# Optimization experiments

Measured on AMD Instinct MI355X. Metric: run time of the kernel, lower is better.

## Reference

```python
import jax, jax.numpy as jnp
import numpy as np

N = 100000
IN_F, C1, C2, C3, OUT_F = 64, 64, 64, 64, 8


def setup_inputs() -> dict:
    key = jax.random.key(0)
    ks = jax.random.split(key, 12)
    x = jax.random.normal(ks[0], (N, IN_F), dtype=jnp.float32)
    edge_index = jax.random.randint(ks[1], (2, 1600000), 0, N, dtype=jnp.int64)

    def lin(kw, kb, fi, fo):
        s = 1.0 / np.sqrt(fi)
        W = jax.random.uniform(kw, (fi, fo), jnp.float32, -s, s)
        b = jax.random.uniform(kb, (fo,), jnp.float32, -s, s)
        return W, b

    W1, b1 = lin(ks[2], ks[3], IN_F, C1)
    W2, b2 = lin(ks[4], ks[5], C1, C2)
    W3, b3 = lin(ks[6], ks[7], C2, C3)
    Wl, bl = lin(ks[8], ks[9], C3, OUT_F)
    return {"x": x, "edge_index": edge_index, "W1": W1, "b1": b1,
            "W2": W2, "b2": b2, "W3": W3, "b3": b3, "Wl": Wl, "bl": bl}


def _gcn_norm(edge_index, n):
    # add self loops, compute symmetric normalization D^-1/2 A D^-1/2
    loops = jnp.arange(n, dtype=edge_index.dtype)
    src = jnp.concatenate([edge_index[0], loops])
    dst = jnp.concatenate([edge_index[1], loops])
    deg = jax.ops.segment_sum(jnp.ones_like(dst, dtype=jnp.float32), dst, num_segments=n)
    dis = jnp.where(deg > 0, jax.lax.rsqrt(deg), 0.0)
    norm = dis[src] * dis[dst]  # [E+N]
    return src, dst, norm


def _gcn_layer(h, W, b, src, dst, norm, n):
    h = h @ W                                   # [N, Fout] small GEMM
    msg = h[src] * norm[:, None]                # gather + scale, [E+N, Fout]
    agg = jax.ops.segment_sum(msg, dst, num_segments=n)  # scatter-add
    return agg + b


def reference(x, edge_index, W1, b1, W2, b2, W3, b3, Wl, bl):
    n = x.shape[0]
    src, dst, norm = _gcn_norm(edge_index, n)
    h = jax.nn.relu(_gcn_layer(x, W1, b1, src, dst, norm, n))
    h = jax.nn.relu(_gcn_layer(h, W2, b2, src, dst, norm, n))
    h = jax.nn.relu(_gcn_layer(h, W3, b3, src, dst, norm, n))
    return h @ Wl + bl
```

## Files before the change

### kernel.cpp

```cpp
#include <hip/hip_runtime.h>
#include <hip/hip_fp16.h>

#define F 64
#define CHUNK 2048
#define BN 512
#define BSHIFT 9
#define CAP 20480

typedef int v4i __attribute__((ext_vector_type(4)));
typedef float v2f __attribute__((ext_vector_type(2)));

__device__ __forceinline__ float rlane(float v, int l) {
    return __uint_as_float(__builtin_amdgcn_readlane(__float_as_uint(v), l));
}

__global__ __launch_bounds__(256) void k_blkcnt(const int* __restrict__ dst,
                                                int* __restrict__ blkcnt,
                                                int E, int NB, int NBKT) {
    __shared__ int lcnt[256];
    int b = blockIdx.x, t = threadIdx.x;
    lcnt[t] = 0;
    __syncthreads();
    const v4i* d4 = (const v4i*)dst;
    int g0 = (b * CHUNK) >> 2;
    int E4 = E >> 2;
#pragma unroll
    for (int k = 0; k < 2; ++k) {
        int gi = g0 + k * 256 + t;
        if (gi < E4) {
            v4i q = __builtin_nontemporal_load(d4 + gi);
            atomicAdd(&lcnt[q.x >> BSHIFT], 1);
            atomicAdd(&lcnt[q.y >> BSHIFT], 1);
            atomicAdd(&lcnt[q.z >> BSHIFT], 1);
            atomicAdd(&lcnt[q.w >> BSHIFT], 1);
        }
    }
    __syncthreads();
    if (t < NBKT) blkcnt[t * NB + b] = lcnt[t];
}

__global__ __launch_bounds__(256) void k_bktscan(const int* __restrict__ blkcnt,
                                                 int* __restrict__ blkoff,
                                                 int* __restrict__ bkttot, int NB) {
    __shared__ int s[256];
    __shared__ int running;
    int seg = blockIdx.x;
    int t = threadIdx.x;
    if (t == 0) running = 0;
    __syncthreads();
    for (int base = 0; base < NB; base += 256) {
        int i = base + t;
        int v = (i < NB) ? blkcnt[seg * NB + i] : 0;
        s[t] = v;
        __syncthreads();
        for (int off = 1; off < 256; off <<= 1) {
            int x = (t >= off) ? s[t - off] : 0;
            __syncthreads();
            s[t] += x;
            __syncthreads();
        }
        int rbase = running;
        if (i < NB) blkoff[seg * NB + i] = rbase + s[t] - v;
        int ctot = s[255];
        __syncthreads();
        if (t == 0) running = rbase + ctot;
        __syncthreads();
    }
    if (t == 0) bkttot[seg] = running;
}

__global__ void k_sb(const int* __restrict__ bkttot, int* __restrict__ sb, int NBKT) {
    __shared__ int s[256];
    int t = threadIdx.x;
    int v = (t < NBKT) ? bkttot[t] : 0;
    s[t] = v;
    __syncthreads();
    for (int off = 1; off < 256; off <<= 1) {
        int x = (t >= off) ? s[t - off] : 0;
        __syncthreads();
        s[t] += x;
        __syncthreads();
    }
    if (t < NBKT) sb[t] = s[t] - v;
    if (t == NBKT - 1) sb[NBKT] = s[t];
}

__global__ __launch_bounds__(256) void k_stage2(const int* __restrict__ src,
                                                const int* __restrict__ dst,
                                                const int* __restrict__ blkoff,
                                                const int* __restrict__ sb,
                                                unsigned* __restrict__ stage,
                                                int E, int NB, int NBKT) {
    __shared__ int lcnt[256];
    __shared__ int lbase[257];
    __shared__ int obase[256];
    __shared__ int s[256];
    __shared__ unsigned rec[CHUNK];
    __shared__ unsigned char binof[CHUNK];
    int b = blockIdx.x, t = threadIdx.x;
    lcnt[t] = 0;
    __syncthreads();
    const v4i* d4 = (const v4i*)dst;
    const v4i* s4 = (const v4i*)src;
    int g0 = (b * CHUNK) >> 2;
    int E4 = E >> 2;
    int myseg[8], myrank[8];
    unsigned myrec[8];
#pragma unroll
    for (int k = 0; k < 2; ++k) {
        int gi = g0 + k * 256 + t;
        bool ok = gi < E4;
        v4i qd = {0, 0, 0, 0}, qs = {0, 0, 0, 0};
        if (ok) {
            qd = __builtin_nontemporal_load(d4 + gi);
            qs = __builtin_nontemporal_load(s4 + gi);
        }
        int dd[4] = {qd.x, qd.y, qd.z, qd.w};
        int ss[4] = {qs.x, qs.y, qs.z, qs.w};
#pragma unroll
        for (int j = 0; j < 4; ++j) {
            int idx = k * 4 + j;
            myseg[idx] = -1;
            if (ok) {
                int sg = dd[j] >> BSHIFT;
                myseg[idx] = sg;
                myrank[idx] = atomicAdd(&lcnt[sg], 1);
                myrec[idx] = ((unsigned)(dd[j] & (BN - 1)) << 17) | (unsigned)ss[j];
            }
        }
    }
    __syncthreads();
    int v = lcnt[t];
    s[t] = v;
    __syncthreads();
    for (int off = 1; off < 256; off <<= 1) {
        int x = (t >= off) ? s[t - off] : 0;
        __syncthreads();
        s[t] += x;
        __syncthreads();
    }
    lbase[t] = s[t] - v;
    if (t == 255) lbase[256] = s[255];
    obase[t] = (t < NBKT) ? sb[t] + blkoff[t * NB + b] : 0;
    __syncthreads();
#pragma unroll
    for (int k = 0; k < 8; ++k) {
        if (myseg[k] >= 0) {
            int p = lbase[myseg[k]] + myrank[k];
            rec[p] = myrec[k];
            binof[p] = (unsigned char)myseg[k];
        }
    }
    __syncthreads();
    int tot = lbase[256];
    for (int j = t; j < tot; j += 256) {
        int sg = binof[j];
        stage[obase[sg] + (j - lbase[sg])] = rec[j];
    }
}

__global__ __launch_bounds__(1024) void k_bincount(const unsigned* __restrict__ stage,
                                                   const int* __restrict__ sb,
                                                   int* __restrict__ count,
                                                   float* __restrict__ dis,
                                                   int* __restrict__ padtot, int n) {
    __shared__ int lc[BN];
    int bkt = blockIdx.x, t = threadIdx.x;
    int nb0 = bkt << BSHIFT;
    if (t < BN) lc[t] = 0;
    __syncthreads();
    int r0 = sb[bkt], r1 = sb[bkt + 1];
    for (int j = r0 + t; j < r1; j += 1024) {
        unsigned r = stage[j];
        atomicAdd(&lc[r >> 17], 1);
    }
    __syncthreads();
    int pv = 0;
    if (t < BN) {
        int node = nb0 + t;
        int cv = lc[t];
        if (node < n) {
            count[node] = cv;
            dis[node] = rsqrtf((float)(cv + 1));
            pv = (cv + 3) & ~3;
        }
    }
    __syncthreads();
    if (t < BN) lc[t] = pv;
    __syncthreads();
    for (int off = 256; off > 0; off >>= 1) {
        if (t < off) lc[t] += lc[t + off];
        __syncthreads();
    }
    if (t == 0) padtot[bkt] = lc[0];
}

__global__ void k_sb2(const int* __restrict__ padtot, int* __restrict__ rbase,
                      int* __restrict__ row_start, int NBKT, int n) {
    __shared__ int s[256];
    int t = threadIdx.x;
    int v = (t < NBKT) ? padtot[t] : 0;
    s[t] = v;
    __syncthreads();
    for (int off = 1; off < 256; off <<= 1) {
        int x = (t >= off) ? s[t - off] : 0;
        __syncthreads();
        s[t] += x;
        __syncthreads();
    }
    if (t < NBKT) rbase[t] = s[t] - v;
    if (t == NBKT - 1) { rbase[NBKT] = s[t]; row_start[n] = s[t]; }
}

__global__ __launch_bounds__(512) void k_binfill(const unsigned* __restrict__ stage,
                                                 const int* __restrict__ sb,
                                                 const int* __restrict__ count,
                                                 const int* __restrict__ rbase,
                                                 int* __restrict__ row_start,
                                                 int* __restrict__ csr, int n) {
    __shared__ int lcur[BN];
    __shared__ int sc[BN];
    __shared__ int buf[CAP];
    int bkt = blockIdx.x, t = threadIdx.x;
    int nb0 = bkt << BSHIFT;
    int node = nb0 + t;
    int pv = (node < n) ? ((count[node] + 3) & ~3) : 0;
    sc[t] = pv;
    __syncthreads();
    for (int off = 1; off < BN; off <<= 1) {
        int x = (t >= off) ? sc[t - off] : 0;
        __syncthreads();
        sc[t] += x;
        __syncthreads();
    }
    int excl = sc[t] - pv;
    int w0 = rbase[bkt];
    int wlen = sc[BN - 1];
    lcur[t] = excl;
    if (node < n) row_start[node] = w0 + excl;
    for (int j = t; j < wlen && j < CAP; j += 512) buf[j] = n;
    __syncthreads();
    int r0 = sb[bkt], r1 = sb[bkt + 1];
    for (int j = r0 + t; j < r1; j += 512) {
        unsigned r = stage[j];
        int p = atomicAdd(&lcur[r >> 17], 1);
        if (p < CAP) buf[p] = (int)(r & 0x1FFFFu);
    }
    __syncthreads();
    for (int j = t; j < wlen && j < CAP; j += 512) csr[w0 + j] = buf[j];
}

__global__ void k_prep(const float4* __restrict__ x4, const float* __restrict__ dis,
                       uint2* __restrict__ hs, uint2* __restrict__ hs2, int n) {
    int i = blockIdx.x * blockDim.x + threadIdx.x;
    int tot = (n + 1) * 16;
    if (i < tot) {
        int row = i >> 4;
        float dv = 0.0f;
        float4 v = make_float4(0.f, 0.f, 0.f, 0.f);
        if (row < n) { dv = dis[row]; v = x4[i]; }
        __half2 h01 = __floats2half2_rn(dv * v.x, dv * v.y);
        __half2 h23 = __floats2half2_rn(dv * v.z, dv * v.w);
        uint2 u;
        u.x = *(unsigned*)&h01;
        u.y = *(unsigned*)&h23;
        hs[i] = u;
    } else if (i < tot + 16) {
        hs2[(size_t)n * 16 + (i - tot)] = make_uint2(0u, 0u);
    }
}

__device__ __forceinline__ void h4acc2(uint2 u, v2f& t01, v2f& t23) {
    float2 fa = __half22float2(*(__half2*)&u.x);
    float2 fb = __half22float2(*(__half2*)&u.y);
    v2f va; va.x = fa.x; va.y = fa.y;
    v2f vb; vb.x = fb.x; vb.y = fb.y;
    t01 += va;
    t23 += vb;
}

__global__ __launch_bounds__(256) void k_layer(const __half* __restrict__ hin,
                                               const float* __restrict__ W,
                                               const float* __restrict__ b,
                                               const int* __restrict__ row_start,
                                               const int* __restrict__ csr,
                                               const float* __restrict__ dis,
                                               __half* __restrict__ hout,
                                               int n, int scale_out) {
    __shared__ float Ws[F * F];
    int tid = threadIdx.x;
#pragma unroll
    for (int i = 0; i < 16; ++i) Ws[tid + i * 256] = W[tid + i * 256];
    __syncthreads();
    int lane = tid & 63;
    int g = lane >> 4;
    int sub = lane & 15;
    int r0 = (blockIdx.x * 4 + (tid >> 6)) * 4;
    if (r0 >= n) return;

    int s0 = row_start[r0];
    int s1 = row_start[r0 + 1];
    int s2 = row_start[r0 + 2];
    int s3 = row_start[r0 + 3];
    int s4 = row_start[r0 + 4];

    v2f a0p[2] = {{0, 0}, {0, 0}};
    v2f a1p[2] = {{0, 0}, {0, 0}};
    v2f a2p[2] = {{0, 0}, {0, 0}};
    v2f a3p[2] = {{0, 0}, {0, 0}};

    const v4i* csr4 = (const v4i*)csr;
    const uint2* h2 = (const uint2*)hin;
    int B0 = s0 >> 2, B4 = s4 >> 2;

    auto ldidx = [&](int bb) -> v4i {
        int mybb = bb + g;
        bool valid = mybb < B4;
        v4i qq = __builtin_nontemporal_load(csr4 + (valid ? mybb : B0));
        if (!valid) { qq.x = n; qq.y = n; qq.z = n; qq.w = n; }
        return qq;
    };

    if (B0 < B4) {
        v4i qcur = ldidx(B0);
        v4i qnxt = (B0 + 4 < B4) ? ldidx(B0 + 4) : qcur;
        uint2 Gc0 = h2[((size_t)qcur.x << 4) + sub];
        uint2 Gc1 = h2[((size_t)qcur.y << 4) + sub];
        uint2 Gc2 = h2[((size_t)qcur.z << 4) + sub];
        uint2 Gc3 = h2[((size_t)qcur.w << 4) + sub];

        for (int bb = B0; bb < B4; bb += 4) {
            bool hasn = bb + 4 < B4;
            uint2 Gn0, Gn1, Gn2, Gn3;
            if (hasn) {
                Gn0 = h2[((size_t)qnxt.x << 4) + sub];
                Gn1 = h2[((size_t)qnxt.y << 4) + sub];
                Gn2 = h2[((size_t)qnxt.z << 4) + sub];
                Gn3 = h2[((size_t)qnxt.w << 4) + sub];
            }
            v4i qn2 = (bb + 8 < B4) ? ldidx(bb + 8) : qnxt;

            int slot = (bb + g) << 2;
            int r = (slot >= s1) + ((slot >= s2) + (slot >= s3));
            v2f t01 = {0, 0}, t23 = {0, 0};
            h4acc2(Gc0, t01, t23);
            h4acc2(Gc1, t01, t23);
            h4acc2(Gc2, t01, t23);
            h4acc2(Gc3, t01, t23);
            float m0 = (r == 0) ? 1.0f : 0.0f;
            float m1 = (r == 1) ? 1.0f : 0.0f;
            float m2 = (r == 2) ? 1.0f : 0.0f;
            float m3 = (r == 3) ? 1.0f : 0.0f;
            a0p[0] = t01 * m0 + a0p[0];
            a0p[1] = t23 * m0 + a0p[1];
            a1p[0] = t01 * m1 + a1p[0];
            a1p[1] = t23 * m1 + a1p[1];
            a2p[0] = t01 * m2 + a2p[0];
            a2p[1] = t23 * m2 + a2p[1];
            a3p[0] = t01 * m3 + a3p[0];
            a3p[1] = t23 * m3 + a3p[1];
            qnxt = qn2;
            if (hasn) { Gc0 = Gn0; Gc1 = Gn1; Gc2 = Gn2; Gc3 = Gn3; }
        }
    }

#pragma unroll
    for (int p = 0; p < 2; ++p) {
        a0p[p].x += __shfl_xor(a0p[p].x, 16); a0p[p].x += __shfl_xor(a0p[p].x, 32);
        a0p[p].y += __shfl_xor(a0p[p].y, 16); a0p[p].y += __shfl_xor(a0p[p].y, 32);
        a1p[p].x += __shfl_xor(a1p[p].x, 16); a1p[p].x += __shfl_xor(a1p[p].x, 32);
        a1p[p].y += __shfl_xor(a1p[p].y, 16); a1p[p].y += __shfl_xor(a1p[p].y, 32);
        a2p[p].x += __shfl_xor(a2p[p].x, 16); a2p[p].x += __shfl_xor(a2p[p].x, 32);
        a2p[p].y += __shfl_xor(a2p[p].y, 16); a2p[p].y += __shfl_xor(a2p[p].y, 32);
        a3p[p].x += __shfl_xor(a3p[p].x, 16); a3p[p].x += __shfl_xor(a3p[p].x, 32);
        a3p[p].y += __shfl_xor(a3p[p].y, 16); a3p[p].y += __shfl_xor(a3p[p].y, 32);
    }

    {
        uint2 u0 = h2[((size_t)(r0 + 0) << 4) + sub];
        uint2 u1 = h2[((size_t)(r0 + 1) << 4) + sub];
        uint2 u2 = h2[((size_t)(r0 + 2) << 4) + sub];
        uint2 u3 = h2[((size_t)(r0 + 3) << 4) + sub];
        h4acc2(u0, a0p[0], a0p[1]);
        h4acc2(u1, a1p[0], a1p[1]);
        h4acc2(u2, a2p[0], a2p[1]);
        h4acc2(u3, a3p[0], a3p[1]);
    }
    float d0 = dis[r0 + 0], d1 = dis[r0 + 1], d2 = dis[r0 + 2], d3 = dis[r0 + 3];
    a0p[0] *= d0; a0p[1] *= d0;
    a1p[0] *= d1; a1p[1] *= d1;
    a2p[0] *= d2; a2p[1] *= d2;
    a3p[0] *= d3; a3p[1] *= d3;

    float bb_ = b[lane];
    v2f ya; ya.x = bb_; ya.y = bb_;
    v2f yb; yb.x = bb_; yb.y = bb_;
#pragma unroll
    for (int a = 0; a < 16; ++a) {
#pragma unroll
        for (int m = 0; m < 4; ++m) {
            float w = Ws[(((a << 2) + m) << 6) + lane];
            v2f rab, rcd;
            rab.x = rlane(a0p[m >> 1][m & 1], a);
            rab.y = rlane(a1p[m >> 1][m & 1], a);
            rcd.x = rlane(a2p[m >> 1][m & 1], a);
            rcd.y = rlane(a3p[m >> 1][m & 1], a);
            ya = rab * w + ya;
            yb = rcd * w + yb;
        }
    }
    float y0 = fmaxf(ya.x, 0.0f);
    float y1 = fmaxf(ya.y, 0.0f);
    float y2 = fmaxf(yb.x, 0.0f);
    float y3 = fmaxf(yb.y, 0.0f);
    if (scale_out) { y0 *= d0; y1 *= d1; y2 *= d2; y3 *= d3; }
    hout[((size_t)(r0 + 0) << 6) + lane] = __float2half(y0);
    hout[((size_t)(r0 + 1) << 6) + lane] = __float2half(y1);
    hout[((size_t)(r0 + 2) << 6) + lane] = __float2half(y2);
    hout[((size_t)(r0 + 3) << 6) + lane] = __float2half(y3);
}

__global__ __launch_bounds__(256) void k_final(const __half* __restrict__ h,
                                               const float* __restrict__ Wl,
                                               const float* __restrict__ bl,
                                               float* __restrict__ out, int n) {
    __shared__ float Ws[F * 8];
    __shared__ float bs[8];
    int tid = threadIdx.x;
    Ws[tid] = Wl[tid];
    Ws[tid + 256] = Wl[tid + 256];
    if (tid < 8) bs[tid] = bl[tid];
    __syncthreads();
    int idx = blockIdx.x * 256 + tid;
    if (idx >= n * 8) return;
    int row = idx >> 3;
    int o = idx & 7;
    const __half* hr = h + (size_t)row * F;
    float acc = bs[o];
#pragma unroll
    for (int k = 0; k < F; ++k) acc = fmaf(__half2float(hr[k]), Ws[k * 8 + o], acc);
    out[idx] = acc;
}

extern "C" void kernel_launch(void* const* d_in, const int* in_sizes, int n_in,
                              void* d_out, int out_size, void* d_ws, size_t ws_size,
                              hipStream_t stream) {
    const float* x  = (const float*)d_in[0];
    const int*   ei = (const int*)d_in[1];
    const float* W1 = (const float*)d_in[2];
    const float* b1 = (const float*)d_in[3];
    const float* W2 = (const float*)d_in[4];
    const float* b2 = (const float*)d_in[5];
    const float* W3 = (const float*)d_in[6];
    const float* b3 = (const float*)d_in[7];
    const float* Wl = (const float*)d_in[8];
    const float* bl = (const float*)d_in[9];
    float* out = (float*)d_out;

    int n = in_sizes[0] / F;
    int E = in_sizes[1] / 2;
    const int* src = ei;
    const int* dst = ei + E;

    int np   = (n + 256) & ~255;
    int cap  = E + 3 * n + 64;
    int NB   = (E + CHUNK - 1) / CHUNK;
    int NBKT = (n + BN - 1) >> BSHIFT;

    int*      count     = (int*)d_ws;
    int*      row_start = count + np;
    int*      blkcnt    = row_start + np;
    int*      blkoff    = blkcnt + 256 * NB;
    int*      bkttot    = blkoff + 256 * NB;
    int*      sb        = bkttot + 256;
    int*      padtot    = sb + 272;
    int*      rbase     = padtot + 256;
    float*    dis       = (float*)(rbase + 272);
    unsigned* stage     = (unsigned*)(dis + np);
    int*      csr       = (int*)(stage + ((E + 3) & ~3));
    __half*   buf1      = (__half*)(csr + ((cap + 3) & ~3));
    __half*   buf2      = buf1 + (size_t)(n + 1) * F;

    k_blkcnt<<<NB, 256, 0, stream>>>(dst, blkcnt, E, NB, NBKT);

    k_bktscan<<<NBKT, 256, 0, stream>>>(blkcnt, blkoff, bkttot, NB);
    k_sb<<<1, 256, 0, stream>>>(bkttot, sb, NBKT);
    k_stage2<<<NB, 256, 0, stream>>>(src, dst, blkoff, sb, stage, E, NB, NBKT);

    k_bincount<<<NBKT, 1024, 0, stream>>>(stage, sb, count, dis, padtot, n);
    k_sb2<<<1, 256, 0, stream>>>(padtot, rbase, row_start, NBKT, n);

    k_binfill<<<NBKT, 512, 0, stream>>>(stage, sb, count, rbase, row_start, csr, n);

    k_prep<<<((n + 1) * 16 + 16 + 255) / 256, 256, 0, stream>>>(
        (const float4*)x, dis, (uint2*)buf1, (uint2*)buf2, n);

    int nb_l = (n / 4 + 3) / 4;
    k_layer<<<nb_l, 256, 0, stream>>>(buf1, W1, b1, row_start, csr, dis, buf2, n, 1);
    k_layer<<<nb_l, 256, 0, stream>>>(buf2, W2, b2, row_start, csr, dis, buf1, n, 1);
    k_layer<<<nb_l, 256, 0, stream>>>(buf1, W3, b3, row_start, csr, dis, buf2, n, 0);

    k_final<<<(n * 8 + 255) / 256, 256, 0, stream>>>(buf2, Wl, bl, out, n);
}
```

Baseline: 283.9 us.

## Aggregate neighbor features with MFMA segment-sum over 16-row wave tiles

Each wave now handles 16 destination rows. It gathers neighbor feature rows in batches of 32 into LDS as an fp16 transposed tile. A 0/1 membership mask matrix then feeds MFMA 16x16x32 instructions, which compute the per-row segment sums; the self loop is folded in as a final identity pass. The dense W transform reads the accumulated tile from LDS with plain FMAs instead of readlane broadcasts. This removes the masked VALU accumulation and shuffle reductions, at the cost of LDS traffic, more padding waste on uneven degrees, and an extra MFMA pass.

```diff
diff --git a/kernel.cpp b/kernel.cpp
--- a/kernel.cpp
+++ b/kernel.cpp
@@ -8,11 +8,10 @@
 #define CAP 20480
 
 typedef int v4i __attribute__((ext_vector_type(4)));
-typedef float v2f __attribute__((ext_vector_type(2)));
-
-__device__ __forceinline__ float rlane(float v, int l) {
-    return __uint_as_float(__builtin_amdgcn_readlane(__float_as_uint(v), l));
-}
+typedef float fx4 __attribute__((ext_vector_type(4)));
+typedef _Float16 h8f __attribute__((ext_vector_type(8)));
+
+union FB8 { uint4 u; h8f h; };
 
 __global__ __launch_bounds__(256) void k_blkcnt(const int* __restrict__ dst,
                                                 int* __restrict__ blkcnt,
@@ -270,154 +269,134 @@
     }
 }
 
-__device__ __forceinline__ void h4acc2(uint2 u, v2f& t01, v2f& t23) {
-    float2 fa = __half22float2(*(__half2*)&u.x);
-    float2 fb = __half22float2(*(__half2*)&u.y);
-    v2f va; va.x = fa.x; va.y = fa.y;
-    v2f vb; vb.x = fb.x; vb.y = fb.y;
-    t01 += va;
-    t23 += vb;
-}
-
 __global__ __launch_bounds__(256) void k_layer(const __half* __restrict__ hin,
-                                               const float* __restrict__ W,
-                                               const float* __restrict__ b,
-                                               const int* __restrict__ row_start,
-                                               const int* __restrict__ csr,
-                                               const float* __restrict__ dis,
-                                               __half* __restrict__ hout,
-                                               int n, int scale_out) {
-    __shared__ float Ws[F * F];
+        const float* __restrict__ W, const float* __restrict__ b,
+        const int* __restrict__ row_start, const int* __restrict__ csr,
+        const float* __restrict__ dis, __half* __restrict__ hout,
+        int n, int scale_out) {
+    __shared__ char lds_all[16384];
     int tid = threadIdx.x;
-#pragma unroll
-    for (int i = 0; i < 16; ++i) Ws[tid + i * 256] = W[tid + i * 256];
-    __syncthreads();
     int lane = tid & 63;
-    int g = lane >> 4;
-    int sub = lane & 15;
-    int r0 = (blockIdx.x * 4 + (tid >> 6)) * 4;
+    int wv = tid >> 6;
+    int r0 = (blockIdx.x * 4 + wv) << 4;
     if (r0 >= n) return;
-
-    int s0 = row_start[r0];
-    int s1 = row_start[r0 + 1];
-    int s2 = row_start[r0 + 2];
-    int s3 = row_start[r0 + 3];
-    int s4 = row_start[r0 + 4];
-
-    v2f a0p[2] = {{0, 0}, {0, 0}};
-    v2f a1p[2] = {{0, 0}, {0, 0}};
-    v2f a2p[2] = {{0, 0}, {0, 0}};
-    v2f a3p[2] = {{0, 0}, {0, 0}};
-
-    const v4i* csr4 = (const v4i*)csr;
-    const uint2* h2 = (const uint2*)hin;
-    int B0 = s0 >> 2, B4 = s4 >> 2;
-
-    auto ldidx = [&](int bb) -> v4i {
-        int mybb = bb + g;
-        bool valid = mybb < B4;
-        v4i qq = __builtin_nontemporal_load(csr4 + (valid ? mybb : B0));
-        if (!valid) { qq.x = n; qq.y = n; qq.z = n; qq.w = n; }
-        return qq;
+    char* myLds = lds_all + (wv << 12);
+    unsigned short* X16 = (unsigned short*)myLds;
+    const uint4* h4 = (const uint4*)hin;
+
+    int r_  = lane & 15;
+    int g4  = lane >> 4;
+    int q32 = lane >> 1;
+    int c2  = lane & 1;
+
+    int lo = row_start[r0 + r_];
+    int hi = row_start[r0 + r_ + 1];
+    int s0 = __shfl(lo, 0);
+    int s4 = __shfl(hi, 15);
+    int NBb = (s4 - s0 + 31) >> 5;
+    unsigned deg = (unsigned)(hi - lo);
+
+    fx4 acc0 = {0.f, 0.f, 0.f, 0.f};
+    fx4 acc1 = acc0, acc2 = acc0, acc3 = acc0;
+
+    auto getnode = [&](int i) -> int {
+        if (i < NBb) {
+            int slot = s0 + (i << 5) + q32;
+            int nd = csr[slot];
+            return (slot < s4) ? nd : n;
+        }
+        return (q32 < 16) ? (r0 + q32) : n;
     };
 
-    if (B0 < B4) {
-        v4i qcur = ldidx(B0);
-        v4i qnxt = (B0 + 4 < B4) ? ldidx(B0 + 4) : qcur;
-        uint2 Gc0 = h2[((size_t)qcur.x << 4) + sub];
-        uint2 Gc1 = h2[((size_t)qcur.y << 4) + sub];
-        uint2 Gc2 = h2[((size_t)qcur.z << 4) + sub];
-        uint2 Gc3 = h2[((size_t)qcur.w << 4) + sub];
-
-        for (int bb = B0; bb < B4; bb += 4) {
-            bool hasn = bb + 4 < B4;
-            uint2 Gn0, Gn1, Gn2, Gn3;
-            if (hasn) {
-                Gn0 = h2[((size_t)qnxt.x << 4) + sub];
-                Gn1 = h2[((size_t)qnxt.y << 4) + sub];
-                Gn2 = h2[((size_t)qnxt.z << 4) + sub];
-                Gn3 = h2[((size_t)qnxt.w << 4) + sub];
-            }
-            v4i qn2 = (bb + 8 < B4) ? ldidx(bb + 8) : qnxt;
-
-            int slot = (bb + g) << 2;
-            int r = (slot >= s1) + ((slot >= s2) + (slot >= s3));
-            v2f t01 = {0, 0}, t23 = {0, 0};
-            h4acc2(Gc0, t01, t23);
-            h4acc2(Gc1, t01, t23);
-            h4acc2(Gc2, t01, t23);
-            h4acc2(Gc3, t01, t23);
-            float m0 = (r == 0) ? 1.0f : 0.0f;
-            float m1 = (r == 1) ? 1.0f : 0.0f;
-            float m2 = (r == 2) ? 1.0f : 0.0f;
-            float m3 = (r == 3) ? 1.0f : 0.0f;
-            a0p[0] = t01 * m0 + a0p[0];
-            a0p[1] = t23 * m0 + a0p[1];
-            a1p[0] = t01 * m1 + a1p[0];
-            a1p[1] = t23 * m1 + a1p[1];
-            a2p[0] = t01 * m2 + a2p[0];
-            a2p[1] = t23 * m2 + a2p[1];
-            a3p[0] = t01 * m3 + a3p[0];
-            a3p[1] = t23 * m3 + a3p[1];
-            qnxt = qn2;
-            if (hasn) { Gc0 = Gn0; Gc1 = Gn1; Gc2 = Gn2; Gc3 = Gn3; }
-        }
-    }
-
-#pragma unroll
-    for (int p = 0; p < 2; ++p) {
-        a0p[p].x += __shfl_xor(a0p[p].x, 16); a0p[p].x += __shfl_xor(a0p[p].x, 32);
-        a0p[p].y += __shfl_xor(a0p[p].y, 16); a0p[p].y += __shfl_xor(a0p[p].y, 32);
-        a1p[p].x += __shfl_xor(a1p[p].x, 16); a1p[p].x += __shfl_xor(a1p[p].x, 32);
-        a1p[p].y += __shfl_xor(a1p[p].y, 16); a1p[p].y += __shfl_xor(a1p[p].y, 32);
-        a2p[p].x += __shfl_xor(a2p[p].x, 16); a2p[p].x += __shfl_xor(a2p[p].x, 32);
-        a2p[p].y += __shfl_xor(a2p[p].y, 16); a2p[p].y += __shfl_xor(a2p[p].y, 32);
-        a3p[p].x += __shfl_xor(a3p[p].x, 16); a3p[p].x += __shfl_xor(a3p[p].x, 32);
-        a3p[p].y += __shfl_xor(a3p[p].y, 16); a3p[p].y += __shfl_xor(a3p[p].y, 32);
-    }
-
-    {
-        uint2 u0 = h2[((size_t)(r0 + 0) << 4) + sub];
-        uint2 u1 = h2[((size_t)(r0 + 1) << 4) + sub];
-        uint2 u2 = h2[((size_t)(r0 + 2) << 4) + sub];
-        uint2 u3 = h2[((size_t)(r0 + 3) << 4) + sub];
-        h4acc2(u0, a0p[0], a0p[1]);
-        h4acc2(u1, a1p[0], a1p[1]);
-        h4acc2(u2, a2p[0], a2p[1]);
-        h4acc2(u3, a3p[0], a3p[1]);
-    }
-    float d0 = dis[r0 + 0], d1 = dis[r0 + 1], d2 = dis[r0 + 2], d3 = dis[r0 + 3];
-    a0p[0] *= d0; a0p[1] *= d0;
-    a1p[0] *= d1; a1p[1] *= d1;
-    a2p[0] *= d2; a2p[1] *= d2;
-    a3p[0] *= d3; a3p[1] *= d3;
+    int nd0 = getnode(0);
+    int ba = nd0 * 8 + c2 * 4;
+    uint4 G0 = h4[ba], G1 = h4[ba + 1], G2 = h4[ba + 2], G3 = h4[ba + 3];
+    int ndn = getnode(1);
+
+    for (int t = 0; t <= NBb; ++t) {
+        int fb = c2 << 5;
+#define PUT(J, GG) { \
+    unsigned short* p = X16 + (((fb + 8 * (J)) << 5) + q32); \
+    p[0]   = (unsigned short)(GG.x); \
+    p[32]  = (unsigned short)(GG.x >> 16); \
+    p[64]  = (unsigned short)(GG.y); \
+    p[96]  = (unsigned short)(GG.y >> 16); \
+    p[128] = (unsigned short)(GG.z); \
+    p[160] = (unsigned short)(GG.z >> 16); \
+    p[192] = (unsigned short)(GG.w); \
+    p[224] = (unsigned short)(GG.w >> 16); \
+}
+        PUT(0, G0) PUT(1, G1) PUT(2, G2) PUT(3, G3)
+#undef PUT
+        if (t < NBb) {
+            int bb = ndn * 8 + c2 * 4;
+            G0 = h4[bb]; G1 = h4[bb + 1]; G2 = h4[bb + 2]; G3 = h4[bb + 3];
+            ndn = getnode(t + 2);
+        }
+        unsigned w[4];
+        if (t < NBb) {
+            unsigned u0 = (unsigned)(s0 + (t << 5) + (g4 << 3)) - (unsigned)lo;
+#pragma unroll
+            for (int jj = 0; jj < 4; ++jj)
+                w[jj] = ((u0 + 2 * jj) < deg ? 0x3C00u : 0u) |
+                        ((u0 + 2 * jj + 1) < deg ? 0x3C000000u : 0u);
+        } else {
+            int k0 = g4 << 3;
+#pragma unroll
+            for (int jj = 0; jj < 4; ++jj)
+                w[jj] = ((k0 + 2 * jj) == r_ ? 0x3C00u : 0u) |
+                        ((k0 + 2 * jj + 1) == r_ ? 0x3C000000u : 0u);
+        }
+        FB8 af; af.u = make_uint4(w[0], w[1], w[2], w[3]);
+        const char* rb = myLds + ((r_ << 6) + (g4 << 4));
+        FB8 b0, b1, b2, b3;
+        b0.u = *(const uint4*)(rb);
+        b1.u = *(const uint4*)(rb + 1024);
+        b2.u = *(const uint4*)(rb + 2048);
+        b3.u = *(const uint4*)(rb + 3072);
+        acc0 = __builtin_amdgcn_mfma_f32_16x16x32_f16(af.h, b0.h, acc0, 0, 0, 0);
+        acc1 = __builtin_amdgcn_mfma_f32_16x16x32_f16(af.h, b1.h, acc1, 0, 0, 0);
+        acc2 = __builtin_amdgcn_mfma_f32_16x16x32_f16(af.h, b2.h, acc2, 0, 0, 0);
+        acc3 = __builtin_amdgcn_mfma_f32_16x16x32_f16(af.h, b3.h, acc3, 0, 0, 0);
+    }
+
+    float* T = (float*)myLds;
+#define TSTORE(S, A) { \
+    int fb_ = ((16 * (S) + r_) << 4) + (g4 << 2); \
+    *(fx4*)(T + fb_) = A; }
+    TSTORE(0, acc0) TSTORE(1, acc1) TSTORE(2, acc2) TSTORE(3, acc3)
+#undef TSTORE
 
     float bb_ = b[lane];
-    v2f ya; ya.x = bb_; ya.y = bb_;
-    v2f yb; yb.x = bb_; yb.y = bb_;
-#pragma unroll
-    for (int a = 0; a < 16; ++a) {
-#pragma unroll
-        for (int m = 0; m < 4; ++m) {
-            float w = Ws[(((a << 2) + m) << 6) + lane];
-            v2f rab, rcd;
-            rab.x = rlane(a0p[m >> 1][m & 1], a);
-            rab.y = rlane(a1p[m >> 1][m & 1], a);
-            rcd.x = rlane(a2p[m >> 1][m & 1], a);
-            rcd.y = rlane(a3p[m >> 1][m & 1], a);
-            ya = rab * w + ya;
-            yb = rcd * w + yb;
-        }
-    }
-    float y0 = fmaxf(ya.x, 0.0f);
-    float y1 = fmaxf(ya.y, 0.0f);
-    float y2 = fmaxf(yb.x, 0.0f);
-    float y3 = fmaxf(yb.y, 0.0f);
-    if (scale_out) { y0 *= d0; y1 *= d1; y2 *= d2; y3 *= d3; }
-    hout[((size_t)(r0 + 0) << 6) + lane] = __float2half(y0);
-    hout[((size_t)(r0 + 1) << 6) + lane] = __float2half(y1);
-    hout[((size_t)(r0 + 2) << 6) + lane] = __float2half(y2);
-    hout[((size_t)(r0 + 3) << 6) + lane] = __float2half(y3);
+    float yv[16];
+#pragma unroll
+    for (int r = 0; r < 16; ++r) yv[r] = 0.f;
+    const float* Wp = W + lane;
+#pragma unroll 4
+    for (int f = 0; f < 64; ++f) {
+        float w = Wp[f << 6];
+        const float* Tf = T + (f << 4);
+        float4 d0 = *(const float4*)(Tf);
+        float4 d1 = *(const float4*)(Tf + 4);
+        float4 d2 = *(const float4*)(Tf + 8);
+        float4 d3 = *(const float4*)(Tf + 12);
+        yv[0]  = fmaf(d0.x, w, yv[0]);  yv[1]  = fmaf(d0.y, w, yv[1]);
+        yv[2]  = fmaf(d0.z, w, yv[2]);  yv[3]  = fmaf(d0.w, w, yv[3]);
+        yv[4]  = fmaf(d1.x, w, yv[4]);  yv[5]  = fmaf(d1.y, w, yv[5]);
+        yv[6]  = fmaf(d1.z, w, yv[6]);  yv[7]  = fmaf(d1.w, w, yv[7]);
+        yv[8]  = fmaf(d2.x, w, yv[8]);  yv[9]  = fmaf(d2.y, w, yv[9]);
+        yv[10] = fmaf(d2.z, w, yv[10]); yv[11] = fmaf(d2.w, w, yv[11]);
+        yv[12] = fmaf(d3.x, w, yv[12]); yv[13] = fmaf(d3.y, w, yv[13]);
+        yv[14] = fmaf(d3.z, w, yv[14]); yv[15] = fmaf(d3.w, w, yv[15]);
+    }
+
+#pragma unroll
+    for (int r = 0; r < 16; ++r) {
+        float dd = dis[r0 + r];
+        float y = fmaxf(yv[r] * dd + bb_, 0.f);
+        if (scale_out) y *= dd;
+        hout[((size_t)(r0 + r) << 6) + lane] = __float2half(y);
+    }
 }
 
 __global__ __launch_bounds__(256) void k_final(const __half* __restrict__ h,
@@ -495,7 +474,7 @@
     k_prep<<<((n + 1) * 16 + 16 + 255) / 256, 256, 0, stream>>>(
         (const float4*)x, dis, (uint2*)buf1, (uint2*)buf2, n);
 
-    int nb_l = (n / 4 + 3) / 4;
+    int nb_l = (n + 63) / 64;
     k_layer<<<nb_l, 256, 0, stream>>>(buf1, W1, b1, row_start, csr, dis, buf2, n, 1);
     k_layer<<<nb_l, 256, 0, stream>>>(buf2, W2, b2, row_start, csr, dis, buf1, n, 1);
     k_layer<<<nb_l, 256, 0, stream>>>(buf1, W3, b3, row_start, csr, dis, buf2, n, 0);
```

Result: faster. 270.9 us (-4.6%).
